# Performance work log

Measured on AMD Instinct MI355X. Metric: run time of the kernel, lower is better.

Reference implementation:

```python
import jax, jax.numpy as jnp
import numpy as np

DEPTH, DIM, HEADS, DIM_HEAD, MLP = 6, 768, 12, 64, 3072
INNER = HEADS * DIM_HEAD  # 768
EPS = 1e-5


def _layernorm(x, w, b):
    m = jnp.mean(x, axis=-1, keepdims=True)
    v = jnp.mean((x - m) ** 2, axis=-1, keepdims=True)
    return (x - m) * jax.lax.rsqrt(v + EPS) * w + b


def setup_inputs() -> dict:
    key = jax.random.key(0)
    ks = jax.random.split(key, 12)
    s = 0.02
    return {
        "x": jax.random.normal(ks[0], (4, 1024, DIM), dtype=jnp.float32),
        "ln1_w": jnp.ones((DEPTH, DIM), jnp.float32),
        "ln1_b": jnp.zeros((DEPTH, DIM), jnp.float32),
        "w_qkv": jax.random.normal(ks[1], (DEPTH, DIM, 3 * INNER), jnp.float32) * s,
        "w_o": jax.random.normal(ks[2], (DEPTH, INNER, DIM), jnp.float32) * s,
        "b_o": jnp.zeros((DEPTH, DIM), jnp.float32),
        "ln2_w": jnp.ones((DEPTH, DIM), jnp.float32),
        "ln2_b": jnp.zeros((DEPTH, DIM), jnp.float32),
        "w1": jax.random.normal(ks[3], (DEPTH, DIM, MLP), jnp.float32) * s,
        "b1": jnp.zeros((DEPTH, MLP), jnp.float32),
        "w2": jax.random.normal(ks[4], (DEPTH, MLP, DIM), jnp.float32) * s,
        "b2": jnp.zeros((DEPTH, DIM), jnp.float32),
    }


def _forward(x, ln1_w, ln1_b, w_qkv, w_o, b_o, ln2_w, ln2_b, w1, b1, w2, b2):
    scale = DIM_HEAD ** -0.5
    b, n, _ = x.shape

    def block(x, p):
        l1w, l1b, wqkv, wo, bo, l2w, l2b, W1, B1, W2, B2 = p
        # --- attention (pre-norm); dropout/droppath are identity in eval ---
        h = _layernorm(x, l1w, l1b)
        qkv = h @ wqkv                                   # [b, n, 3*inner]
        q, k, v = jnp.split(qkv, 3, axis=-1)
        q = q.reshape(b, n, HEADS, DIM_HEAD).transpose(0, 2, 1, 3)
        k = k.reshape(b, n, HEADS, DIM_HEAD).transpose(0, 2, 1, 3)
        v = v.reshape(b, n, HEADS, DIM_HEAD).transpose(0, 2, 1, 3)
        dots = jnp.einsum('bhid,bhjd->bhij', q, k) * scale   # [b, h, n, n]
        attn = jax.nn.softmax(dots, axis=-1)
        out = jnp.einsum('bhij,bhjd->bhid', attn, v)
        out = out.transpose(0, 2, 1, 3).reshape(b, n, INNER)
        x = x + out @ wo + bo
        # --- feed-forward (pre-norm), exact GELU like torch default ---
        h = _layernorm(x, l2w, l2b)
        x = x + jax.nn.gelu(h @ W1 + B1, approximate=False) @ W2 + B2
        return x, None

    x, _ = jax.lax.scan(block, x, (ln1_w, ln1_b, w_qkv, w_o, b_o,
                                   ln2_w, ln2_b, w1, b1, w2, b2))
    return x


def reference(x, ln1_w, ln1_b, w_qkv, w_o, b_o, ln2_w, ln2_b, w1, b1, w2, b2):
    return _forward(x, ln1_w, ln1_b, w_qkv, w_o, b_o, ln2_w, ln2_b, w1, b1, w2, b2)
```

## Files before the change

### kernel.cpp

```cpp
#include <hip/hip_runtime.h>
#include <cmath>
#include <cstdint>

typedef __bf16 bf16_t;
typedef __bf16 bf16x8 __attribute__((ext_vector_type(8)));
typedef __bf16 bf16x4 __attribute__((ext_vector_type(4)));
typedef float  f32x4  __attribute__((ext_vector_type(4)));

#define DEPTH 6
#define DIM   768
#define HEADS 12
#define DH    64
#define MLPD  3072
#define SEQ   1024
#define BATCH 4
#define MTOT  (BATCH*SEQ)
#define QKVN  2304

static __device__ __forceinline__ bf16x8 ld8(const bf16_t* p) {
    return *(const bf16x8*)p;
}

typedef const __attribute__((address_space(1))) unsigned int gas_u32;
typedef __attribute__((address_space(3))) unsigned int las_u32;
static __device__ __forceinline__ void gload16(const bf16_t* g, bf16_t* l) {
    __builtin_amdgcn_global_load_lds((gas_u32*)g, (las_u32*)l, 16, 0, 0);
}

__global__ __launch_bounds__(256) void tcvt_kernel(const float* __restrict__ in,
                                                   bf16_t* __restrict__ out,
                                                   int K, int N) {
    __shared__ float ts[32][33];
    int n0 = blockIdx.x * 32, k0 = blockIdx.y * 32;
    size_t base = (size_t)blockIdx.z * K * N;
    int tx = threadIdx.x & 31, ty = threadIdx.x >> 5;
    #pragma unroll
    for (int r = 0; r < 32; r += 8)
        ts[ty + r][tx] = in[base + (size_t)(k0 + ty + r) * N + n0 + tx];
    __syncthreads();
    #pragma unroll
    for (int r = 0; r < 32; r += 8)
        out[base + (size_t)(n0 + ty + r) * K + k0 + tx] = (bf16_t)ts[tx][ty + r];
}

__global__ __launch_bounds__(192) void lnr_kernel(const float* __restrict__ xin,
                                                  float* __restrict__ xout,
                                                  const float* __restrict__ P,
                                                  int nslices,
                                                  const float* __restrict__ bias,
                                                  const float* __restrict__ w,
                                                  const float* __restrict__ b,
                                                  bf16_t* __restrict__ h,
                                                  int writeLN) {
    int row = blockIdx.x, t = threadIdx.x;
    size_t r4 = (size_t)row * 192 + t;
    float4 v = ((const float4*)xin)[r4];
    if (nslices) {
        float4 bi = ((const float4*)bias)[t];
        v.x += bi.x; v.y += bi.y; v.z += bi.z; v.w += bi.w;
        for (int s = 0; s < nslices; s++) {
            float4 pv = ((const float4*)P)[(size_t)s * MTOT * 192 + r4];
            v.x += pv.x; v.y += pv.y; v.z += pv.z; v.w += pv.w;
        }
        ((float4*)xout)[r4] = v;
    }
    float s = v.x + v.y + v.z + v.w;
    float q = v.x * v.x + v.y * v.y + v.z * v.z + v.w * v.w;
    #pragma unroll
    for (int off = 32; off > 0; off >>= 1) {
        s += __shfl_down(s, off);
        q += __shfl_down(q, off);
    }
    __shared__ float ss[3], sq[3], stat[2];
    if ((t & 63) == 0) { ss[t >> 6] = s; sq[t >> 6] = q; }
    __syncthreads();
    if (t == 0) {
        float S = ss[0] + ss[1] + ss[2];
        float Q = sq[0] + sq[1] + sq[2];
        float mean = S * (1.0f / DIM);
        float var  = Q * (1.0f / DIM) - mean * mean;
        stat[0] = mean;
        stat[1] = rsqrtf(var + 1e-5f);
    }
    __syncthreads();
    if (writeLN) {
        float mean = stat[0], rstd = stat[1];
        float4 wv4 = ((const float4*)w)[t];
        float4 bv4 = ((const float4*)b)[t];
        bf16x4 o;
        o[0] = (bf16_t)((v.x - mean) * rstd * wv4.x + bv4.x);
        o[1] = (bf16_t)((v.y - mean) * rstd * wv4.y + bv4.y);
        o[2] = (bf16_t)((v.z - mean) * rstd * wv4.z + bv4.z);
        o[3] = (bf16_t)((v.w - mean) * rstd * wv4.w + bv4.w);
        *(bf16x4*)&h[(size_t)row * DIM + t * 4] = o;
    }
}

template <int EPI>
__global__ __launch_bounds__(512) void gemm_kernel(const bf16_t* __restrict__ A,
                                                   const bf16_t* __restrict__ Bt,
                                                   const float* __restrict__ bias,
                                                   bf16_t* __restrict__ Cb,
                                                   float* __restrict__ Cf,
                                                   bf16_t* __restrict__ Vt,
                                                   int N, int K, int klen) {
    __shared__ __align__(16) bf16_t As[2][256 * 32];
    __shared__ __align__(16) bf16_t Bs[2][64 * 32];
    int t = threadIdx.x;
    int NX = gridDim.x;
    int flat = blockIdx.y * NX + blockIdx.x;
    int jj = flat >> 3;
    int bxs = jj % NX;
    int bys = (flat & 7) + ((jj / NX) << 3);
    int m0 = bys * 256, n0 = bxs * 64;
    int kz = blockIdx.z;
    int kbeg = kz * klen;
    int lane = t & 63, l16 = lane & 15, quad = lane >> 4;
    int wv = t >> 6;
    int wm = wv >> 1, wn = wv & 1;
    f32x4 acc[4][2] = {};

    int sr = lane >> 2;
    int sc = ((lane & 3) ^ ((lane >> 3) & 3)) * 8;
    const bf16_t* gA0 = A  + (size_t)(m0 + wv * 32 + sr) * K + sc;
    const bf16_t* gA1 = gA0 + (size_t)16 * K;
    const bf16_t* gB0 = Bt + (size_t)(n0 + (wv & 3) * 16 + sr) * K + sc;
    bf16_t* lA0 = &As[0][(wv * 32) * 32];
    bf16_t* lA1 = &As[0][(wv * 32 + 16) * 32];
    bf16_t* lB0 = &Bs[0][((wv & 3) * 16) * 32];
    constexpr int bufA = 256 * 32;
    constexpr int bufB = 64 * 32;

    auto stage = [&](int buf, int k0) {
        gload16(gA0 + k0, lA0 + buf * bufA);
        gload16(gA1 + k0, lA1 + buf * bufA);
        if (wv < 4) gload16(gB0 + k0, lB0 + buf * bufB);
    };

    int nIt = klen >> 5;
    stage(0, kbeg);
    int posA = (quad ^ ((l16 >> 1) & 3)) * 8;

    for (int it = 0; it < nIt; it++) {
        __syncthreads();
        if (it + 1 < nIt) stage((it + 1) & 1, kbeg + (it + 1) * 32);
        const bf16_t* as = As[it & 1];
        const bf16_t* bs = Bs[it & 1];
        bf16x8 af[4], bfr[2];
        #pragma unroll
        for (int i = 0; i < 4; i++)
            af[i] = ld8(&as[(wm * 64 + i * 16 + l16) * 32 + posA]);
        #pragma unroll
        for (int j = 0; j < 2; j++)
            bfr[j] = ld8(&bs[(wn * 32 + j * 16 + l16) * 32 + posA]);
        #pragma unroll
        for (int i = 0; i < 4; i++)
            #pragma unroll
            for (int j = 0; j < 2; j++)
                acc[i][j] = __builtin_amdgcn_mfma_f32_16x16x32_bf16(af[i], bfr[j], acc[i][j], 0, 0, 0);
    }

    if constexpr (EPI == 0) {
        if (n0 >= 1536) {
            int b = m0 >> 10;
            #pragma unroll
            for (int i = 0; i < 4; i++) {
                int n = (m0 & 1023) + wm * 64 + i * 16 + quad * 4;
                #pragma unroll
                for (int j = 0; j < 2; j++) {
                    int hc = n0 + wn * 32 + j * 16 + l16 - 1536;
                    int hh = hc >> 6, d = hc & 63;
                    bf16x4 ov;
                    #pragma unroll
                    for (int r = 0; r < 4; r++) ov[r] = (bf16_t)acc[i][j][r];
                    *(bf16x4*)&Vt[(((size_t)b * HEADS + hh) * 64 + d) * SEQ + n] = ov;
                }
            }
            return;
        }
    }
    #pragma unroll
    for (int i = 0; i < 4; i++) {
        int grow = m0 + wm * 64 + i * 16 + quad * 4;
        #pragma unroll
        for (int j = 0; j < 2; j++) {
            int gcol = n0 + wn * 32 + j * 16 + l16;
            float bv = 0.0f;
            if constexpr (EPI == 1) bv = bias[gcol];
            #pragma unroll
            for (int r = 0; r < 4; r++) {
                size_t idx = (size_t)(grow + r) * N + gcol;
                float v = acc[i][j][r];
                if constexpr (EPI == 0) {
                    Cb[idx] = (bf16_t)v;
                } else if constexpr (EPI == 1) {
                    v += bv;
                    v = 0.5f * v * (1.0f + erff(v * 0.70710678118654752f));
                    Cb[idx] = (bf16_t)v;
                } else {
                    Cf[(size_t)kz * MTOT * N + idx] = v;
                }
            }
        }
    }
}

__global__ __launch_bounds__(256) void attn_kernel(const bf16_t* __restrict__ qkv,
                                                   const bf16_t* __restrict__ vt,
                                                   bf16_t* __restrict__ out) {
    int flat = (blockIdx.z * gridDim.y + blockIdx.y) * gridDim.x + blockIdx.x;
    int jj = flat >> 3;
    int qt = jj & 15;
    int bh = (flat & 7) + ((jj >> 4) << 3);
    int h = bh % HEADS, b = bh / HEADS;
    int t = threadIdx.x;
    int wv = t >> 6, lane = t & 63, l16 = lane & 15, quad = lane >> 4;
    const float LOG2E = 1.44269504f;
    int qw0 = qt * 64 + wv * 16;

    __shared__ __align__(16) bf16_t Ks[2][64 * 64];
    __shared__ __align__(16) bf16_t Vs[2][64 * 64];
    __shared__ __align__(16) bf16_t Pa[4][16 * 72];
    bf16_t* P = Pa[wv];

    size_t bS = (size_t)b * SEQ;
    const bf16_t* qrow = qkv + (bS + qw0 + l16) * QKVN + h * 64;
    bf16x8 qf0 = ld8(qrow + quad * 8);
    bf16x8 qf1 = ld8(qrow + 32 + quad * 8);

    float m = -3e38f, l = 0.0f;
    f32x4 o[4] = {};

    const bf16_t* kbase = qkv + bS * QKVN + 768 + h * 64;
    const bf16_t* vbase = vt + ((size_t)(b * HEADS + h) * 64) * SEQ;

    int ar = lane >> 3;
    int ac = ((lane & 7) ^ ar) * 8;
    int i0 = wv * 2, i1 = wv * 2 + 1;
    const bf16_t* gK0 = kbase + (size_t)(i0 * 8 + ar) * QKVN + ac;
    const bf16_t* gK1 = kbase + (size_t)(i1 * 8 + ar) * QKVN + ac;
    const bf16_t* gV0 = vbase + (size_t)(i0 * 8 + ar) * SEQ + ac;
    const bf16_t* gV1 = vbase + (size_t)(i1 * 8 + ar) * SEQ + ac;

    auto stage = [&](int buf, int kb) {
        gload16(gK0 + (size_t)kb * QKVN, &Ks[buf][i0 * 8 * 64]);
        gload16(gK1 + (size_t)kb * QKVN, &Ks[buf][i1 * 8 * 64]);
        gload16(gV0 + kb, &Vs[buf][i0 * 8 * 64]);
        gload16(gV1 + kb, &Vs[buf][i1 * 8 * 64]);
    };

    stage(0, 0);
    int p0 = (quad ^ (l16 & 7)) * 8;
    int p1 = ((quad + 4) ^ (l16 & 7)) * 8;

    for (int it = 0; it < SEQ / 64; it++) {
        __syncthreads();
        if (it + 1 < SEQ / 64) stage((it + 1) & 1, (it + 1) * 64);
        const bf16_t* ks = Ks[it & 1];
        const bf16_t* vs = Vs[it & 1];

        f32x4 s[4];
        #pragma unroll
        for (int tt = 0; tt < 4; tt++) {
            const bf16_t* kr = &ks[(tt * 16 + l16) * 64];
            f32x4 z = {};
            z = __builtin_amdgcn_mfma_f32_16x16x32_bf16(ld8(kr + p0), qf0, z, 0, 0, 0);
            z = __builtin_amdgcn_mfma_f32_16x16x32_bf16(ld8(kr + p1), qf1, z, 0, 0, 0);
            s[tt] = z;
        }
        float mx = -3e38f;
        #pragma unroll
        for (int tt = 0; tt < 4; tt++)
            #pragma unroll
            for (int r = 0; r < 4; r++) {
                s[tt][r] *= 0.125f;
                mx = fmaxf(mx, s[tt][r]);
            }
        mx = fmaxf(mx, __shfl_xor(mx, 16));
        mx = fmaxf(mx, __shfl_xor(mx, 32));
        float mn = fmaxf(m, mx);
        float alpha = exp2f((m - mn) * LOG2E);
        m = mn;
        float nb = mn * LOG2E;
        float rs = 0.0f;
        #pragma unroll
        for (int tt = 0; tt < 4; tt++) {
            bf16x4 pkt;
            #pragma unroll
            for (int r = 0; r < 4; r++) {
                float p = exp2f(fmaf(s[tt][r], LOG2E, -nb));
                rs += p;
                pkt[r] = (bf16_t)p;
            }
            *(bf16x4*)&P[l16 * 72 + tt * 16 + quad * 4] = pkt;
        }
        l = l * alpha + rs;
        #pragma unroll
        for (int jt = 0; jt < 4; jt++) o[jt] *= alpha;
        asm volatile("s_waitcnt lgkmcnt(0)" ::: "memory");
        bf16x8 pf0 = ld8(&P[l16 * 72 + quad * 8]);
        bf16x8 pf1 = ld8(&P[l16 * 72 + 32 + quad * 8]);
        #pragma unroll
        for (int jt = 0; jt < 4; jt++) {
            const bf16_t* vr = &vs[(jt * 16 + l16) * 64];
            o[jt] = __builtin_amdgcn_mfma_f32_16x16x32_bf16(ld8(vr + p0), pf0, o[jt], 0, 0, 0);
            o[jt] = __builtin_amdgcn_mfma_f32_16x16x32_bf16(ld8(vr + p1), pf1, o[jt], 0, 0, 0);
        }
    }

    l += __shfl_xor(l, 16);
    l += __shfl_xor(l, 32);
    float inv = 1.0f / l;
    bf16_t* orow = out + (bS + qw0 + l16) * DIM + h * 64;
    #pragma unroll
    for (int jt = 0; jt < 4; jt++) {
        bf16x4 ov;
        #pragma unroll
        for (int r = 0; r < 4; r++) ov[r] = (bf16_t)(o[jt][r] * inv);
        *(bf16x4*)&orow[jt * 16 + quad * 4] = ov;
    }
}

extern "C" void kernel_launch(void* const* d_in, const int* in_sizes, int n_in,
                              void* d_out, int out_size, void* d_ws, size_t ws_size,
                              hipStream_t stream) {
    const float* x     = (const float*)d_in[0];
    const float* ln1_w = (const float*)d_in[1];
    const float* ln1_b = (const float*)d_in[2];
    const float* w_qkv = (const float*)d_in[3];
    const float* w_o   = (const float*)d_in[4];
    const float* b_o   = (const float*)d_in[5];
    const float* ln2_w = (const float*)d_in[6];
    const float* ln2_b = (const float*)d_in[7];
    const float* w1    = (const float*)d_in[8];
    const float* b1    = (const float*)d_in[9];
    const float* w2    = (const float*)d_in[10];
    const float* b2    = (const float*)d_in[11];
    float* out = (float*)d_out;

    char* ws = (char*)d_ws;
    size_t off = 0;
    auto alloc = [&](size_t bytes) -> char* {
        char* p = ws + off;
        off += (bytes + 255) & ~(size_t)255;
        return p;
    };
    bf16_t* wqkv_t = (bf16_t*)alloc((size_t)DEPTH * DIM * QKVN * 2);
    bf16_t* wo_t   = (bf16_t*)alloc((size_t)DEPTH * DIM * DIM * 2);
    bf16_t* w1_t   = (bf16_t*)alloc((size_t)DEPTH * DIM * MLPD * 2);
    bf16_t* w2_t   = (bf16_t*)alloc((size_t)DEPTH * MLPD * DIM * 2);
    bf16_t* hbuf   = (bf16_t*)alloc((size_t)MTOT * DIM * 2);
    bf16_t* qkvb   = (bf16_t*)alloc((size_t)MTOT * QKVN * 2);
    bf16_t* vtb    = (bf16_t*)alloc((size_t)BATCH * HEADS * 64 * SEQ * 2);
    bf16_t* aob    = (bf16_t*)alloc((size_t)MTOT * DIM * 2);
    bf16_t* midb   = (bf16_t*)alloc((size_t)MTOT * MLPD * 2);
    float*  Pm     = (float*)alloc((size_t)4 * MTOT * DIM * 4);
    float*  Pp     = (float*)qkvb;
    if (off > ws_size) return;

    tcvt_kernel<<<dim3(QKVN / 32, DIM / 32, DEPTH), 256, 0, stream>>>(w_qkv, wqkv_t, DIM, QKVN);
    tcvt_kernel<<<dim3(DIM / 32,  DIM / 32, DEPTH), 256, 0, stream>>>(w_o,   wo_t,   DIM, DIM);
    tcvt_kernel<<<dim3(MLPD / 32, DIM / 32, DEPTH), 256, 0, stream>>>(w1,    w1_t,   DIM, MLPD);
    tcvt_kernel<<<dim3(DIM / 32, MLPD / 32, DEPTH), 256, 0, stream>>>(w2,    w2_t,   MLPD, DIM);

    hipMemcpyAsync(out, x, (size_t)MTOT * DIM * 4, hipMemcpyDeviceToDevice, stream);

    lnr_kernel<<<MTOT, 192, 0, stream>>>(out, out, nullptr, 0, nullptr,
                                         ln1_w, ln1_b, hbuf, 1);

    for (int L = 0; L < DEPTH; L++) {
        gemm_kernel<0><<<dim3(QKVN / 64, MTOT / 256, 1), 512, 0, stream>>>(
            hbuf, wqkv_t + (size_t)L * DIM * QKVN, nullptr, qkvb, nullptr, vtb,
            QKVN, DIM, DIM);
        attn_kernel<<<dim3(SEQ / 64, HEADS, BATCH), 256, 0, stream>>>(qkvb, vtb, aob);
        gemm_kernel<2><<<dim3(DIM / 64, MTOT / 256, 2), 512, 0, stream>>>(
            aob, wo_t + (size_t)L * DIM * DIM, nullptr, nullptr, Pp, nullptr,
            DIM, DIM, 384);
        lnr_kernel<<<MTOT, 192, 0, stream>>>(out, out, Pp, 2, b_o + L * DIM,
                                             ln2_w + L * DIM, ln2_b + L * DIM, hbuf, 1);
        gemm_kernel<1><<<dim3(MLPD / 64, MTOT / 256, 1), 512, 0, stream>>>(
            hbuf, w1_t + (size_t)L * DIM * MLPD, b1 + L * MLPD, midb, nullptr, nullptr,
            MLPD, DIM, DIM);
        gemm_kernel<2><<<dim3(DIM / 64, MTOT / 256, 4), 512, 0, stream>>>(
            midb, w2_t + (size_t)L * MLPD * DIM, nullptr, nullptr, Pm, nullptr,
            DIM, MLPD, 768);
        if (L < DEPTH - 1) {
            lnr_kernel<<<MTOT, 192, 0, stream>>>(out, out, Pm, 4, b2 + L * DIM,
                                                 ln1_w + (L + 1) * DIM,
                                                 ln1_b + (L + 1) * DIM, hbuf, 1);
        } else {
            lnr_kernel<<<MTOT, 192, 0, stream>>>(out, out, Pm, 4, b2 + L * DIM,
                                                 ln1_w, ln1_b, hbuf, 0);
        }
    }
}
```

Measured before the change: 1.311 ms.

## Accumulate split-K GEMM partials atomically into residual; one-wave-per-row layernorm

The split-K projection and MLP2 GEMMs now atomically add their fp32 partials straight into the residual buffer, replacing writes to separate partial-sum slices that the layernorm kernel later read back and summed. The proj GEMM's split rises from 2 to 4. The layernorm kernel now handles one row per wavefront with four rows per block, doing the reduction with xor shuffles and dropping the shared-memory syncs. This cuts the partial-buffer traffic, but adds atomic contention on the output and makes the summation order nondeterministic.

After: 1.561 ms. +19.1%, slower.

```diff
diff --git a/kernel.cpp b/kernel.cpp
--- a/kernel.cpp
+++ b/kernel.cpp
@@ -43,67 +43,62 @@
         out[base + (size_t)(n0 + ty + r) * K + k0 + tx] = (bf16_t)ts[tx][ty + r];
 }
 
-__global__ __launch_bounds__(192) void lnr_kernel(const float* __restrict__ xin,
-                                                  float* __restrict__ xout,
-                                                  const float* __restrict__ P,
-                                                  int nslices,
+__global__ __launch_bounds__(256) void lnr_kernel(float* __restrict__ x,
                                                   const float* __restrict__ bias,
                                                   const float* __restrict__ w,
                                                   const float* __restrict__ b,
                                                   bf16_t* __restrict__ h,
                                                   int writeLN) {
-    int row = blockIdx.x, t = threadIdx.x;
-    size_t r4 = (size_t)row * 192 + t;
-    float4 v = ((const float4*)xin)[r4];
-    if (nslices) {
-        float4 bi = ((const float4*)bias)[t];
-        v.x += bi.x; v.y += bi.y; v.z += bi.z; v.w += bi.w;
-        for (int s = 0; s < nslices; s++) {
-            float4 pv = ((const float4*)P)[(size_t)s * MTOT * 192 + r4];
-            v.x += pv.x; v.y += pv.y; v.z += pv.z; v.w += pv.w;
-        }
-        ((float4*)xout)[r4] = v;
-    }
-    float s = v.x + v.y + v.z + v.w;
-    float q = v.x * v.x + v.y * v.y + v.z * v.z + v.w * v.w;
+    int lane = threadIdx.x & 63;
+    int row = blockIdx.x * 4 + (threadIdx.x >> 6);
+    float4* xr = (float4*)(x + (size_t)row * DIM);
+    float4 v0 = xr[lane], v1 = xr[lane + 64], v2 = xr[lane + 128];
+    if (bias) {
+        const float4* bi = (const float4*)bias;
+        float4 c0 = bi[lane], c1 = bi[lane + 64], c2 = bi[lane + 128];
+        v0.x += c0.x; v0.y += c0.y; v0.z += c0.z; v0.w += c0.w;
+        v1.x += c1.x; v1.y += c1.y; v1.z += c1.z; v1.w += c1.w;
+        v2.x += c2.x; v2.y += c2.y; v2.z += c2.z; v2.w += c2.w;
+        xr[lane] = v0; xr[lane + 64] = v1; xr[lane + 128] = v2;
+    }
+    float s = v0.x + v0.y + v0.z + v0.w + v1.x + v1.y + v1.z + v1.w
+            + v2.x + v2.y + v2.z + v2.w;
+    float q = v0.x * v0.x + v0.y * v0.y + v0.z * v0.z + v0.w * v0.w
+            + v1.x * v1.x + v1.y * v1.y + v1.z * v1.z + v1.w * v1.w
+            + v2.x * v2.x + v2.y * v2.y + v2.z * v2.z + v2.w * v2.w;
     #pragma unroll
     for (int off = 32; off > 0; off >>= 1) {
-        s += __shfl_down(s, off);
-        q += __shfl_down(q, off);
-    }
-    __shared__ float ss[3], sq[3], stat[2];
-    if ((t & 63) == 0) { ss[t >> 6] = s; sq[t >> 6] = q; }
-    __syncthreads();
-    if (t == 0) {
-        float S = ss[0] + ss[1] + ss[2];
-        float Q = sq[0] + sq[1] + sq[2];
-        float mean = S * (1.0f / DIM);
-        float var  = Q * (1.0f / DIM) - mean * mean;
-        stat[0] = mean;
-        stat[1] = rsqrtf(var + 1e-5f);
-    }
-    __syncthreads();
+        s += __shfl_xor(s, off);
+        q += __shfl_xor(q, off);
+    }
+    float mean = s * (1.0f / DIM);
+    float rstd = rsqrtf(q * (1.0f / DIM) - mean * mean + 1e-5f);
     if (writeLN) {
-        float mean = stat[0], rstd = stat[1];
-        float4 wv4 = ((const float4*)w)[t];
-        float4 bv4 = ((const float4*)b)[t];
-        bf16x4 o;
-        o[0] = (bf16_t)((v.x - mean) * rstd * wv4.x + bv4.x);
-        o[1] = (bf16_t)((v.y - mean) * rstd * wv4.y + bv4.y);
-        o[2] = (bf16_t)((v.z - mean) * rstd * wv4.z + bv4.z);
-        o[3] = (bf16_t)((v.w - mean) * rstd * wv4.w + bv4.w);
-        *(bf16x4*)&h[(size_t)row * DIM + t * 4] = o;
+        const float4* w4 = (const float4*)w;
+        const float4* b4 = (const float4*)b;
+        bf16_t* hr = h + (size_t)row * DIM;
+        float4 vv[3] = {v0, v1, v2};
+        #pragma unroll
+        for (int k = 0; k < 3; k++) {
+            float4 wv = w4[lane + 64 * k], bv = b4[lane + 64 * k];
+            bf16x4 o;
+            o[0] = (bf16_t)((vv[k].x - mean) * rstd * wv.x + bv.x);
+            o[1] = (bf16_t)((vv[k].y - mean) * rstd * wv.y + bv.y);
+            o[2] = (bf16_t)((vv[k].z - mean) * rstd * wv.z + bv.z);
+            o[3] = (bf16_t)((vv[k].w - mean) * rstd * wv.w + bv.w);
+            *(bf16x4*)&hr[(lane + 64 * k) * 4] = o;
+        }
     }
 }
 
 template <int EPI>
-__global__ __launch_bounds__(512) void gemm_kernel(const bf16_t* __restrict__ A,
-                                                   const bf16_t* __restrict__ Bt,
-                                                   const float* __restrict__ bias,
-                                                   bf16_t* __restrict__ Cb,
-                                                   float* __restrict__ Cf,
-                                                   bf16_t* __restrict__ Vt,
-                                                   int N, int K, int klen) {
+static __device__ __forceinline__ void gemm_body(const bf16_t* __restrict__ A,
+                                                 const bf16_t* __restrict__ Bt,
+                                                 const float* __restrict__ bias,
+                                                 bf16_t* __restrict__ Cb,
+                                                 float* __restrict__ Co,
+                                                 bf16_t* __restrict__ Vt,
+                                                 int N, int K, int klen) {
     __shared__ __align__(16) bf16_t As[2][256 * 32];
     __shared__ __align__(16) bf16_t Bs[2][64 * 32];
     int t = threadIdx.x;
@@ -198,11 +193,34 @@
                     v = 0.5f * v * (1.0f + erff(v * 0.70710678118654752f));
                     Cb[idx] = (bf16_t)v;
                 } else {
-                    Cf[(size_t)kz * MTOT * N + idx] = v;
+                    atomicAdd(&Co[idx], v);
                 }
             }
         }
     }
+}
+
+__global__ __launch_bounds__(512) void qkv_gemm(const bf16_t* __restrict__ A,
+                                                const bf16_t* __restrict__ Bt,
+                                                bf16_t* __restrict__ Cb,
+                                                bf16_t* __restrict__ Vt) {
+    gemm_body<0>(A, Bt, nullptr, Cb, nullptr, Vt, QKVN, DIM, DIM);
+}
+__global__ __launch_bounds__(512) void proj_gemm(const bf16_t* __restrict__ A,
+                                                 const bf16_t* __restrict__ Bt,
+                                                 float* __restrict__ Co) {
+    gemm_body<2>(A, Bt, nullptr, nullptr, Co, nullptr, DIM, DIM, 192);
+}
+__global__ __launch_bounds__(512) void mlp1_gemm(const bf16_t* __restrict__ A,
+                                                 const bf16_t* __restrict__ Bt,
+                                                 const float* __restrict__ bias,
+                                                 bf16_t* __restrict__ Cb) {
+    gemm_body<1>(A, Bt, bias, Cb, nullptr, nullptr, MLPD, DIM, DIM);
+}
+__global__ __launch_bounds__(512) void mlp2_gemm(const bf16_t* __restrict__ A,
+                                                 const bf16_t* __restrict__ Bt,
+                                                 float* __restrict__ Co) {
+    gemm_body<2>(A, Bt, nullptr, nullptr, Co, nullptr, DIM, MLPD, 768);
 }
 
 __global__ __launch_bounds__(256) void attn_kernel(const bf16_t* __restrict__ qkv,
@@ -354,8 +372,6 @@
     bf16_t* vtb    = (bf16_t*)alloc((size_t)BATCH * HEADS * 64 * SEQ * 2);
     bf16_t* aob    = (bf16_t*)alloc((size_t)MTOT * DIM * 2);
     bf16_t* midb   = (bf16_t*)alloc((size_t)MTOT * MLPD * 2);
-    float*  Pm     = (float*)alloc((size_t)4 * MTOT * DIM * 4);
-    float*  Pp     = (float*)qkvb;
     if (off > ws_size) return;
 
     tcvt_kernel<<<dim3(QKVN / 32, DIM / 32, DEPTH), 256, 0, stream>>>(w_qkv, wqkv_t, DIM, QKVN);
@@ -365,32 +381,28 @@
 
     hipMemcpyAsync(out, x, (size_t)MTOT * DIM * 4, hipMemcpyDeviceToDevice, stream);
 
-    lnr_kernel<<<MTOT, 192, 0, stream>>>(out, out, nullptr, 0, nullptr,
-                                         ln1_w, ln1_b, hbuf, 1);
+    lnr_kernel<<<MTOT / 4, 256, 0, stream>>>(out, nullptr, ln1_w, ln1_b, hbuf, 1);
 
     for (int L = 0; L < DEPTH; L++) {
-        gemm_kernel<0><<<dim3(QKVN / 64, MTOT / 256, 1), 512, 0, stream>>>(
-            hbuf, wqkv_t + (size_t)L * DIM * QKVN, nullptr, qkvb, nullptr, vtb,
-            QKVN, DIM, DIM);
+        qkv_gemm<<<dim3(QKVN / 64, MTOT / 256, 1), 512, 0, stream>>>(
+            hbuf, wqkv_t + (size_t)L * DIM * QKVN, qkvb, vtb);
         attn_kernel<<<dim3(SEQ / 64, HEADS, BATCH), 256, 0, stream>>>(qkvb, vtb, aob);
-        gemm_kernel<2><<<dim3(DIM / 64, MTOT / 256, 2), 512, 0, stream>>>(
-            aob, wo_t + (size_t)L * DIM * DIM, nullptr, nullptr, Pp, nullptr,
-            DIM, DIM, 384);
-        lnr_kernel<<<MTOT, 192, 0, stream>>>(out, out, Pp, 2, b_o + L * DIM,
-                                             ln2_w + L * DIM, ln2_b + L * DIM, hbuf, 1);
-        gemm_kernel<1><<<dim3(MLPD / 64, MTOT / 256, 1), 512, 0, stream>>>(
-            hbuf, w1_t + (size_t)L * DIM * MLPD, b1 + L * MLPD, midb, nullptr, nullptr,
-            MLPD, DIM, DIM);
-        gemm_kernel<2><<<dim3(DIM / 64, MTOT / 256, 4), 512, 0, stream>>>(
-            midb, w2_t + (size_t)L * MLPD * DIM, nullptr, nullptr, Pm, nullptr,
-            DIM, MLPD, 768);
+        proj_gemm<<<dim3(DIM / 64, MTOT / 256, 4), 512, 0, stream>>>(
+            aob, wo_t + (size_t)L * DIM * DIM, out);
+        lnr_kernel<<<MTOT / 4, 256, 0, stream>>>(out, b_o + L * DIM,
+                                                 ln2_w + L * DIM, ln2_b + L * DIM,
+                                                 hbuf, 1);
+        mlp1_gemm<<<dim3(MLPD / 64, MTOT / 256, 1), 512, 0, stream>>>(
+            hbuf, w1_t + (size_t)L * DIM * MLPD, b1 + L * MLPD, midb);
+        mlp2_gemm<<<dim3(DIM / 64, MTOT / 256, 4), 512, 0, stream>>>(
+            midb, w2_t + (size_t)L * MLPD * DIM, out);
         if (L < DEPTH - 1) {
-            lnr_kernel<<<MTOT, 192, 0, stream>>>(out, out, Pm, 4, b2 + L * DIM,
-                                                 ln1_w + (L + 1) * DIM,
-                                                 ln1_b + (L + 1) * DIM, hbuf, 1);
+            lnr_kernel<<<MTOT / 4, 256, 0, stream>>>(out, b2 + L * DIM,
+                                                     ln1_w + (L + 1) * DIM,
+                                                     ln1_b + (L + 1) * DIM, hbuf, 1);
         } else {
-            lnr_kernel<<<MTOT, 192, 0, stream>>>(out, out, Pm, 4, b2 + L * DIM,
-                                                 ln1_w, ln1_b, hbuf, 0);
-        }
-    }
-}
+            lnr_kernel<<<MTOT / 4, 256, 0, stream>>>(out, b2 + L * DIM,
+                                                     nullptr, nullptr, nullptr, 0);
+        }
+    }
+}
```
